# Kernel tuning notes

Hardware: AMD Instinct MI355X
Metric: run time of the kernel (lower is better)

Reference implementation:

```python
import jax, jax.numpy as jnp
import numpy as np
import math

# Config (matches init_kwargs)
H, SQK, PQK, SV, PV = 12, 16, 4, 16, 8
C1, C2 = 384, 128
NR, NA = 512, 256
N = NR + NA
WC = math.sqrt(2.0 / (9.0 * PQK))
WL = math.sqrt(1.0 / 3.0)


def quat_to_rot(q):
    # q: [..., 4] (w, x, y, z); normalize then build rotation matrix [..., 3, 3]
    q = q / jnp.linalg.norm(q, axis=-1, keepdims=True)
    w, x, y, z = q[..., 0], q[..., 1], q[..., 2], q[..., 3]
    return jnp.stack([
        jnp.stack([1 - 2 * (y * y + z * z), 2 * (x * y - w * z), 2 * (x * z + w * y)], -1),
        jnp.stack([2 * (x * y + w * z), 1 - 2 * (x * x + z * z), 2 * (y * z - w * x)], -1),
        jnp.stack([2 * (x * z - w * y), 2 * (y * z + w * x), 1 - 2 * (x * x + y * y)], -1),
    ], -2)


def setup_inputs() -> dict:
    key = jax.random.key(0)
    ks = jax.random.split(key, 16)
    s = 0.02
    return {
        'rec_1d': jax.random.normal(ks[0], (1, NR, C1), jnp.float32),
        'lig_1d': jax.random.normal(ks[1], (1, NA, C1), jnp.float32),
        'rep_2d': jax.random.normal(ks[2], (1, N, N, C2), jnp.float32),
        'rec_T': jax.random.normal(ks[3], (1, NR, 7), jnp.float32),
        'lig_T': jax.random.normal(ks[4], (1, NA, 7), jnp.float32),
        'rec_w1d': jax.random.normal(ks[5], (C1, (2 * SQK + SV) * H), jnp.float32) * s,
        'rec_wpt': jax.random.normal(ks[6], (C1, (2 * PQK + PV) * H * 3), jnp.float32) * s,
        'lig_w1d': jax.random.normal(ks[7], (C1, (2 * SQK + SV) * H), jnp.float32) * s,
        'lig_wpt': jax.random.normal(ks[8], (C1, (2 * PQK + PV) * H * 3), jnp.float32) * s,
        'rr_w': jax.random.normal(ks[9], (C2, H), jnp.float32) * s,
        'll_w': jax.random.normal(ks[10], (C2, H), jnp.float32) * s,
        'rl_w': jax.random.normal(ks[11], (C2, H), jnp.float32) * s,
        'lr_w': jax.random.normal(ks[12], (C2, H), jnp.float32) * s,
        'final_w': jax.random.normal(ks[13], (H * (C2 + SV + 4 * PV), C1), jnp.float32) * s,
        'final_b': jnp.zeros((C1,), jnp.float32),
    }


def reference(rec_1d, lig_1d, rep_2d, rec_T, lig_T, rec_w1d, rec_wpt, lig_w1d, lig_wpt,
              rr_w, ll_w, rl_w, lr_w, final_w, final_b):
    B = rec_1d.shape[0]

    def scalar_kqv(x, w, n):
        kqv = (x @ w).reshape(B, n, H, 2 * SQK + SV)
        return kqv[..., :SQK], kqv[..., SQK:2 * SQK], kqv[..., 2 * SQK:]

    rec_k1, rec_q1, rec_v1 = scalar_kqv(rec_1d, rec_w1d, NR)
    lig_k1, lig_q1, lig_v1 = scalar_kqv(lig_1d, lig_w1d, NA)

    # 2d pair biases per block: [B, i, j, H]
    rr = rep_2d[:, :NR, :NR] @ rr_w
    ll = rep_2d[:, NR:, NR:] @ ll_w
    rl = rep_2d[:, :NR, NR:] @ rl_w
    lr = rep_2d[:, NR:, :NR] @ lr_w

    def point_kqv(x, w, T, n):
        R = quat_to_rot(T[..., :4])          # [B, n, 3, 3]
        t = T[..., 4:]                        # [B, n, 3]
        local = (x @ w).reshape(B, n, 3, H * (2 * PQK + PV))
        glob = jnp.einsum('bnij,bnjd->bnid', R, local) + t[..., None]
        glob = glob.reshape(B, n, 3, H, 2 * PQK + PV)
        return glob[..., :PQK], glob[..., PQK:2 * PQK], glob[..., 2 * PQK:], R, t

    rec_kp, rec_qp, rec_vp, rec_R, rec_t = point_kqv(rec_1d, rec_wpt, rec_T, NR)
    lig_kp, lig_qp, lig_vp, lig_R, lig_t = point_kqv(lig_1d, lig_wpt, lig_T, NA)

    q_point = jnp.concatenate([rec_qp, lig_qp], axis=1)  # [B, N, 3, H, PQK]
    k_point = jnp.concatenate([rec_kp, lig_kp], axis=1)

    # squared distances summed over xyz and points -> [B, N, N, H]
    diff = q_point[:, :, None] - k_point[:, None, :]     # [B, N, N, 3, H, PQK]
    d2 = jnp.sum(jnp.square(diff), axis=3).sum(axis=-1)
    aff = -WC * d2

    bias = jnp.concatenate([
        jnp.concatenate([rr, rl], axis=2),
        jnp.concatenate([lr, ll], axis=2),
    ], axis=1)
    aff = aff + bias

    q1 = jnp.concatenate([rec_q1, lig_q1], axis=1)
    k1 = jnp.concatenate([rec_k1, lig_k1], axis=1)
    aff = aff + (WL / math.sqrt(SQK)) * jnp.einsum('bihc,bjhc->bijh', q1, k1)

    weights = jax.nn.softmax(aff, axis=2)  # [B, N, N, H]

    # 2d aggregation: [B, N, H, C2]
    o_2d = jnp.einsum('bijh,bijc->bihc', weights, rep_2d).reshape(B, N, H * C2)

    # scalar-v term: faithful to source (v_1d.unsqueeze(2) broadcasts over j,
    # so it reduces to v_1d * sum_j weights)
    v_1d = jnp.concatenate([rec_v1, lig_v1], axis=1)     # [B, N, H, SV]
    o_1d = (v_1d * jnp.sum(weights, axis=2)[..., None]).reshape(B, N, H * SV)

    # point-v aggregation in global frame: [B, N, 3, PV, H]
    v_point = jnp.concatenate([rec_vp, lig_vp], axis=1)  # [B, N, 3, H, PV]
    out_global = jnp.einsum('bijh,bjdhp->bidph', weights, v_point)

    def invert(glob, R, t):
        return jnp.einsum('bnji,bnjph->bniph', R, glob - t[..., None, None])

    out_local = jnp.concatenate([
        invert(out_global[:, :NR], rec_R, rec_t),
        invert(out_global[:, NR:], lig_R, lig_t),
    ], axis=1)                                           # [B, N, 3, PV, H]
    out_local = jnp.transpose(out_local, (0, 1, 3, 4, 2))  # [B, N, PV, H, 3]
    o_pt = out_local.reshape(B, N, PV * H * 3)
    o_norm = jnp.sqrt(jnp.sum(jnp.square(out_local), axis=-1)).reshape(B, N, PV * H)

    feat = jnp.concatenate([o_2d, o_1d, o_pt, o_norm], axis=-1)
    return feat @ final_w + final_b
```

## Files before the change

### kernel.cpp

```cpp
#include <hip/hip_runtime.h>
#include <math.h>

#define H_   12
#define NRR  512
#define N_   768
#define C1_  384
#define C2_  128
static __device__ __constant__ float WC_  = 0.2357022603955158f;
static __device__ __constant__ float SC1_ = 0.14433756729740646f;

#define OFF_Q1   0
#define OFF_QP   147456
#define OFF_V1   258048
#define OFF_VP   405504
#define OFF_R    626688
#define OFF_T    633600
#define OFF_KHAT 635904
#define OFF_W    930816
#define OFF_FEAT 8008704
#define OFF_PART 9630720

__global__ __launch_bounds__(192) void proj_kernel(
    const float* __restrict__ rec_1d, const float* __restrict__ lig_1d,
    const float* __restrict__ rec_T,  const float* __restrict__ lig_T,
    const float* __restrict__ rec_w1d, const float* __restrict__ rec_wpt,
    const float* __restrict__ lig_w1d, const float* __restrict__ lig_wpt,
    float* __restrict__ ws) {
  const int tok0 = blockIdx.x * 4;
  const int tid  = threadIdx.x;
  __shared__ float xs[4][384];
  __shared__ float loc[4][576];
  __shared__ float Rs[4][9];
  __shared__ float tts[4][3];

  for (int r = 0; r < 4; ++r) {
    int n = tok0 + r;
    const float* x = (n < NRR) ? rec_1d + n * C1_ : lig_1d + (n - NRR) * C1_;
    for (int k = tid; k < C1_; k += 192) xs[r][k] = x[k];
  }
  if (tid < 4) {
    int n = tok0 + tid;
    const float* T = (n < NRR) ? rec_T + n * 7 : lig_T + (n - NRR) * 7;
    float qw = T[0], qx = T[1], qy = T[2], qz = T[3];
    float inv = 1.0f / sqrtf(qw*qw + qx*qx + qy*qy + qz*qz);
    qw *= inv; qx *= inv; qy *= inv; qz *= inv;
    Rs[tid][0] = 1.f - 2.f*(qy*qy + qz*qz);
    Rs[tid][1] = 2.f*(qx*qy - qw*qz);
    Rs[tid][2] = 2.f*(qx*qz + qw*qy);
    Rs[tid][3] = 2.f*(qx*qy + qw*qz);
    Rs[tid][4] = 1.f - 2.f*(qx*qx + qz*qz);
    Rs[tid][5] = 2.f*(qy*qz - qw*qx);
    Rs[tid][6] = 2.f*(qx*qz - qw*qy);
    Rs[tid][7] = 2.f*(qy*qz + qw*qx);
    Rs[tid][8] = 1.f - 2.f*(qx*qx + qy*qy);
    tts[tid][0] = T[4]; tts[tid][1] = T[5]; tts[tid][2] = T[6];
    float* Rg = ws + OFF_R + n * 9;
    #pragma unroll
    for (int k = 0; k < 9; ++k) Rg[k] = Rs[tid][k];
    float* tg = ws + OFF_T + n * 3;
    tg[0] = T[4]; tg[1] = T[5]; tg[2] = T[6];
  }
  __syncthreads();

  const float* w1 = (tok0 < NRR) ? rec_w1d : lig_w1d;
  const float* w2 = (tok0 < NRR) ? rec_wpt : lig_wpt;
  for (int cc = 0; cc < 3; ++cc) {
    int c = tid + cc * 192;
    float a0=0,a1=0,a2=0,a3=0,b0=0,b1=0,b2=0,b3=0;
    for (int k = 0; k < C1_; ++k) {
      float wv = w1[k * 576 + c];
      float wp = w2[k * 576 + c];
      float x0 = xs[0][k], x1 = xs[1][k], x2 = xs[2][k], x3 = xs[3][k];
      a0 += x0*wv; a1 += x1*wv; a2 += x2*wv; a3 += x3*wv;
      b0 += x0*wp; b1 += x1*wp; b2 += x2*wp; b3 += x3*wp;
    }
    loc[0][c]=b0; loc[1][c]=b1; loc[2][c]=b2; loc[3][c]=b3;
    int h = c / 48, e = c % 48;
    float av[4] = {a0,a1,a2,a3};
    for (int r = 0; r < 4; ++r) {
      int n = tok0 + r;
      if (e < 16)      ws[OFF_KHAT + ((size_t)h*N_ + n)*32 + e] = av[r];
      else if (e < 32) ws[OFF_Q1 + n*192 + h*16 + (e-16)]       = av[r];
      else             ws[OFF_V1 + n*192 + h*16 + (e-32)]       = av[r];
    }
  }
  __syncthreads();

  {
    int cp = tid;
    int h = cp >> 4, e = cp & 15;
    for (int r = 0; r < 4; ++r) {
      int n = tok0 + r;
      float g[3];
      #pragma unroll
      for (int d = 0; d < 3; ++d)
        g[d] = Rs[r][d*3+0]*loc[r][cp] + Rs[r][d*3+1]*loc[r][192+cp]
             + Rs[r][d*3+2]*loc[r][384+cp] + tts[r][d];
      if (e < 4) {
        #pragma unroll
        for (int d = 0; d < 3; ++d)
          ws[OFF_KHAT + ((size_t)h*N_ + n)*32 + 16 + e*3 + d] = g[d];
      } else if (e < 8) {
        #pragma unroll
        for (int d = 0; d < 3; ++d) ws[OFF_QP + n*144 + h*12 + (e-4)*3 + d] = g[d];
      } else {
        #pragma unroll
        for (int d = 0; d < 3; ++d) ws[OFF_VP + n*288 + d*96 + h*8 + (e-8)] = g[d];
      }
    }
  }
}

__global__ __launch_bounds__(256) void bias_kernel(
    const float* __restrict__ rep, const float* __restrict__ rr_w,
    const float* __restrict__ ll_w, const float* __restrict__ rl_w,
    const float* __restrict__ lr_w, float* __restrict__ wsW) {
  const int bx = blockIdx.x;
  const int i = bx / 12, jc = bx % 12;
  const int j0 = jc * 64;
  const int t = threadIdx.x;
  __shared__ float lds[64*128];
  __shared__ float wlw[12*128];
  const float* Wq = (i < NRR) ? ((j0 < NRR) ? rr_w : rl_w)
                              : ((j0 < NRR) ? lr_w : ll_w);
  for (int idx = t; idx < 1536; idx += 256) {
    int h = idx >> 7, c = idx & 127;
    wlw[idx] = Wq[c*12 + h];
  }
  const float* src = rep + ((size_t)i*N_ + j0) * C2_;
  for (int idx = t; idx < 2048; idx += 256) {
    int j = idx >> 5, c4 = idx & 31;
    float4 v = *(const float4*)(src + j*128 + c4*4);
    *(float4*)&lds[j*128 + ((c4 ^ j) & 31) * 4] = v;
  }
  __syncthreads();
  const int j = t & 63, hg = t >> 6;
  const int jx = j & 31;
  float a0 = 0.f, a1 = 0.f, a2 = 0.f;
  const float* w0p = wlw + hg*128;
  const float* w1p = wlw + (hg+4)*128;
  const float* w2p = wlw + (hg+8)*128;
  #pragma unroll 8
  for (int c4 = 0; c4 < 32; ++c4) {
    float4 d  = *(const float4*)&lds[j*128 + ((c4 ^ jx) << 2)];
    float4 w0 = *(const float4*)&w0p[c4*4];
    float4 w1 = *(const float4*)&w1p[c4*4];
    float4 w2 = *(const float4*)&w2p[c4*4];
    a0 += d.x*w0.x + d.y*w0.y + d.z*w0.z + d.w*w0.w;
    a1 += d.x*w1.x + d.y*w1.y + d.z*w1.z + d.w*w1.w;
    a2 += d.x*w2.x + d.y*w2.y + d.z*w2.z + d.w*w2.w;
  }
  wsW[((size_t)i*12 + hg    )*N_ + j0 + j] = a0;
  wsW[((size_t)i*12 + hg + 4)*N_ + j0 + j] = a1;
  wsW[((size_t)i*12 + hg + 8)*N_ + j0 + j] = a2;
}

__global__ __launch_bounds__(256) void attn_kernel(float* ws) {
  const int i = blockIdx.x / H_;
  const int h = blockIdx.x % H_;
  const int tid = threadIdx.x;
  float q1v[16], qpv[12];
  #pragma unroll
  for (int c = 0; c < 16; c += 4)
    *(float4*)&q1v[c] = *(const float4*)(ws + OFF_Q1 + i*192 + h*16 + c);
  #pragma unroll
  for (int c = 0; c < 12; c += 4)
    *(float4*)&qpv[c] = *(const float4*)(ws + OFF_QP + i*144 + h*12 + c);

  float* wrow = ws + OFF_W + ((size_t)i*H_ + h) * N_;
  float aff[3];
  #pragma unroll
  for (int r = 0; r < 3; ++r) {
    int j = tid + r*256;
    const float* khf = ws + OFF_KHAT + ((size_t)h*N_ + j)*32;
    float kv[28];
    #pragma unroll
    for (int c = 0; c < 28; c += 4) *(float4*)&kv[c] = *(const float4*)(khf + c);
    float s = 0.f;
    #pragma unroll
    for (int c = 0; c < 16; ++c) s += q1v[c] * kv[c];
    float d2 = 0.f;
    #pragma unroll
    for (int c = 0; c < 12; ++c) { float df = qpv[c] - kv[16+c]; d2 += df*df; }
    aff[r] = wrow[j] + SC1_*s - WC_*d2;
  }
  float m = fmaxf(fmaxf(aff[0], aff[1]), aff[2]);
  #pragma unroll
  for (int off = 32; off; off >>= 1) m = fmaxf(m, __shfl_xor(m, off));
  __shared__ float redm[4], reds[4];
  int wid = tid >> 6, lane = tid & 63;
  if (lane == 0) redm[wid] = m;
  __syncthreads();
  m = fmaxf(fmaxf(redm[0], redm[1]), fmaxf(redm[2], redm[3]));
  float e0 = __expf(aff[0]-m), e1 = __expf(aff[1]-m), e2 = __expf(aff[2]-m);
  float ssum = e0 + e1 + e2;
  #pragma unroll
  for (int off = 32; off; off >>= 1) ssum += __shfl_xor(ssum, off);
  if (lane == 0) reds[wid] = ssum;
  __syncthreads();
  float invs = 1.0f / (reds[0] + reds[1] + reds[2] + reds[3]);
  wrow[tid      ] = e0 * invs;
  wrow[tid + 256] = e1 * invs;
  wrow[tid + 512] = e2 * invs;
}

__global__ __launch_bounds__(256) void o2d_kernel(
    const float* __restrict__ rep, const float* __restrict__ w,
    float* __restrict__ feat) {
  const int i = blockIdx.x;
  const int t = threadIdx.x;
  __shared__ float wl[N_ * H_];
  for (int idx = t; idx < 2304; idx += 256) {
    float4 g = *(const float4*)(w + (size_t)i*9216 + idx*4);
    int h = idx / 192, j4 = idx % 192;
    wl[(j4*4+0)*12 + h] = g.x;
    wl[(j4*4+1)*12 + h] = g.y;
    wl[(j4*4+2)*12 + h] = g.z;
    wl[(j4*4+3)*12 + h] = g.w;
  }
  __syncthreads();
  const int c4 = t & 31, jg = t >> 5;
  float acc[48];
  #pragma unroll
  for (int k = 0; k < 48; ++k) acc[k] = 0.f;
  const float* rrow = rep + (size_t)i * N_ * C2_;
  #pragma unroll 4
  for (int j = jg; j < N_; j += 8) {
    float4 v = *(const float4*)(rrow + j*128 + c4*4);
    float4 wa = *(const float4*)&wl[j*12];
    float4 wb = *(const float4*)&wl[j*12 + 4];
    float4 wc = *(const float4*)&wl[j*12 + 8];
    float wv[12] = {wa.x,wa.y,wa.z,wa.w, wb.x,wb.y,wb.z,wb.w, wc.x,wc.y,wc.z,wc.w};
    #pragma unroll
    for (int hh = 0; hh < 12; ++hh) {
      acc[hh*4+0] += v.x*wv[hh];
      acc[hh*4+1] += v.y*wv[hh];
      acc[hh*4+2] += v.z*wv[hh];
      acc[hh*4+3] += v.w*wv[hh];
    }
  }
  #pragma unroll
  for (int k = 0; k < 48; ++k) acc[k] += __shfl_xor(acc[k], 32);
  const int wave = t >> 6, lane = t & 63;
  __syncthreads();
  if (wave >= 2 && lane < 32) {
    float* dst = wl + (wave-2)*1536 + lane*48;
    #pragma unroll
    for (int k = 0; k < 48; ++k) dst[k] = acc[k];
  }
  __syncthreads();
  if (wave < 2 && lane < 32) {
    const float* s2 = wl + wave*1536 + lane*48;
    #pragma unroll
    for (int k = 0; k < 48; ++k) acc[k] += s2[k];
  }
  __syncthreads();
  if (wave == 1 && lane < 32) {
    float* dst = wl + lane*48;
    #pragma unroll
    for (int k = 0; k < 48; ++k) dst[k] = acc[k];
  }
  __syncthreads();
  if (wave == 0 && lane < 32) {
    const float* s2 = wl + lane*48;
    #pragma unroll
    for (int k = 0; k < 48; ++k) acc[k] += s2[k];
    #pragma unroll
    for (int hh = 0; hh < 12; ++hh) {
      float4 r;
      r.x = acc[hh*4+0]; r.y = acc[hh*4+1]; r.z = acc[hh*4+2]; r.w = acc[hh*4+3];
      *(float4*)&feat[(size_t)i*2112 + hh*128 + lane*4] = r;
    }
  }
}

__global__ __launch_bounds__(320) void opoint_kernel(
    const float* __restrict__ w, const float* __restrict__ vp,
    const float* __restrict__ R, const float* __restrict__ tvec,
    const float* __restrict__ v1, float* __restrict__ feat) {
  const int i = blockIdx.x;
  const int tid = threadIdx.x;
  __shared__ float wl[H_ * N_];
  __shared__ float og[288];
  __shared__ float ol[288];
  for (int k = tid; k < H_*N_; k += 320) wl[k] = w[(size_t)i*H_*N_ + k];
  __syncthreads();
  if (tid < 288) {
    int d = tid / 96, hh = (tid % 96) / 8;
    float acc = 0.f;
    for (int j = 0; j < N_; ++j) acc += wl[hh*N_ + j] * vp[(size_t)j*288 + tid];
    og[tid] = acc - tvec[i*3 + d];
  }
  if (tid < 192) feat[(size_t)i*2112 + 1536 + tid] = v1[(size_t)i*192 + tid];
  __syncthreads();
  if (tid < 288) {
    int i3 = tid / 96, rem = tid % 96, hh = rem / 8, p = rem % 8;
    float o = R[i*9 + 0*3 + i3] * og[0*96 + rem]
            + R[i*9 + 1*3 + i3] * og[1*96 + rem]
            + R[i*9 + 2*3 + i3] * og[2*96 + rem];
    ol[tid] = o;
    feat[(size_t)i*2112 + 1728 + p*36 + hh*3 + i3] = o;
  }
  __syncthreads();
  if (tid < 96) {
    int hh = tid / 8, p = tid % 8;
    float a = ol[0*96 + tid], b = ol[1*96 + tid], c = ol[2*96 + tid];
    feat[(size_t)i*2112 + 2016 + p*12 + hh] = sqrtf(a*a + b*b + c*c);
  }
}

__global__ __launch_bounds__(384) void final1_kernel(
    const float* __restrict__ ws, const float* __restrict__ fw,
    float* __restrict__ part) {
  const int i0 = blockIdx.x * 4;
  const int ks = blockIdx.y;
  const int o  = threadIdx.x;
  const int k0 = ks * 1056;
  __shared__ float fl[4 * 1056];
  const float* feat = ws + OFF_FEAT;
  for (int idx = o; idx < 1056; idx += 384) {
    int r = idx / 264, f4 = idx % 264;
    *(float4*)&fl[r*1056 + f4*4] =
        *(const float4*)(feat + (size_t)(i0+r)*2112 + k0 + f4*4);
  }
  __syncthreads();
  float a0=0,a1=0,a2=0,a3=0;
  for (int f4 = 0; f4 < 264; ++f4) {
    int f = k0 + f4*4;
    float w0 = fw[(size_t)(f+0)*384 + o];
    float w1 = fw[(size_t)(f+1)*384 + o];
    float w2 = fw[(size_t)(f+2)*384 + o];
    float w3 = fw[(size_t)(f+3)*384 + o];
    float4 f0 = *(const float4*)&fl[0*1056 + f4*4];
    float4 f1 = *(const float4*)&fl[1*1056 + f4*4];
    float4 f2 = *(const float4*)&fl[2*1056 + f4*4];
    float4 f3 = *(const float4*)&fl[3*1056 + f4*4];
    a0 += f0.x*w0 + f0.y*w1 + f0.z*w2 + f0.w*w3;
    a1 += f1.x*w0 + f1.y*w1 + f1.z*w2 + f1.w*w3;
    a2 += f2.x*w0 + f2.y*w1 + f2.z*w2 + f2.w*w3;
    a3 += f3.x*w0 + f3.y*w1 + f3.z*w2 + f3.w*w3;
  }
  part[((size_t)ks*N_ + i0+0)*384 + o] = a0;
  part[((size_t)ks*N_ + i0+1)*384 + o] = a1;
  part[((size_t)ks*N_ + i0+2)*384 + o] = a2;
  part[((size_t)ks*N_ + i0+3)*384 + o] = a3;
}

__global__ __launch_bounds__(256) void final2_kernel(
    const float* __restrict__ part, const float* __restrict__ fb,
    float* __restrict__ out) {
  int idx = blockIdx.x * 256 + threadIdx.x;
  int col = idx % 384;
  out[idx] = part[idx] + part[294912 + idx] + fb[col];
}

extern "C" void kernel_launch(void* const* d_in, const int* in_sizes, int n_in,
                              void* d_out, int out_size, void* d_ws, size_t ws_size,
                              hipStream_t stream) {
  const float* rec_1d  = (const float*)d_in[0];
  const float* lig_1d  = (const float*)d_in[1];
  const float* rep_2d  = (const float*)d_in[2];
  const float* rec_T   = (const float*)d_in[3];
  const float* lig_T   = (const float*)d_in[4];
  const float* rec_w1d = (const float*)d_in[5];
  const float* rec_wpt = (const float*)d_in[6];
  const float* lig_w1d = (const float*)d_in[7];
  const float* lig_wpt = (const float*)d_in[8];
  const float* rr_w    = (const float*)d_in[9];
  const float* ll_w    = (const float*)d_in[10];
  const float* rl_w    = (const float*)d_in[11];
  const float* lr_w    = (const float*)d_in[12];
  const float* final_w = (const float*)d_in[13];
  const float* final_b = (const float*)d_in[14];
  float* ws  = (float*)d_ws;
  float* out = (float*)d_out;

  proj_kernel<<<192, 192, 0, stream>>>(rec_1d, lig_1d, rec_T, lig_T,
                                       rec_w1d, rec_wpt, lig_w1d, lig_wpt, ws);
  bias_kernel<<<N_*12, 256, 0, stream>>>(rep_2d, rr_w, ll_w, rl_w, lr_w,
                                         ws + OFF_W);
  attn_kernel<<<N_*H_, 256, 0, stream>>>(ws);
  o2d_kernel<<<N_, 256, 0, stream>>>(rep_2d, ws + OFF_W, ws + OFF_FEAT);
  opoint_kernel<<<N_, 320, 0, stream>>>(ws + OFF_W, ws + OFF_VP, ws + OFF_R,
                                        ws + OFF_T, ws + OFF_V1, ws + OFF_FEAT);
  final1_kernel<<<dim3(N_/4, 2), 384, 0, stream>>>(ws, final_w, ws + OFF_PART);
  final2_kernel<<<1152, 256, 0, stream>>>(ws + OFF_PART, final_b, out);
}
```

Baseline: 863.9 us.

## Fuse bias, softmax and o2d into a single-pass flash-style kernel with bf16 MFMA

New measurement: 986.6 us. 14.2% more time.

```diff
diff --git a/kernel.cpp b/kernel.cpp
--- a/kernel.cpp
+++ b/kernel.cpp
@@ -9,16 +9,32 @@
 static __device__ __constant__ float WC_  = 0.2357022603955158f;
 static __device__ __constant__ float SC1_ = 0.14433756729740646f;
 
-#define OFF_Q1   0
-#define OFF_QP   147456
-#define OFF_V1   258048
-#define OFF_VP   405504
-#define OFF_R    626688
-#define OFF_T    633600
-#define OFF_KHAT 635904
-#define OFF_W    930816
-#define OFF_FEAT 8008704
-#define OFF_PART 9630720
+#define OFF_Q1     0
+#define OFF_QP     147456
+#define OFF_V1     258048
+#define OFF_VP     405504
+#define OFF_R      626688
+#define OFF_T      633600
+#define OFF_KHAT   635904
+#define OFF_WFRAG  930816
+#define OFF_QKF    934912
+#define OFF_MUSED  10372096
+#define OFF_MSFIN  10519552
+#define OFF_W      10544128
+#define OFF_FEAT   17622016
+#define OFF_PART   19244032
+
+typedef __attribute__((ext_vector_type(8))) short short8_m;
+typedef __attribute__((ext_vector_type(4))) float f32x4_m;
+
+__device__ __forceinline__ ushort f2bf(float f) {
+  uint u = __float_as_uint(f);
+  uint r = (u + 0x7fffu + ((u >> 16) & 1u)) >> 16;
+  return (ushort)r;
+}
+__device__ __forceinline__ float bf2f(ushort v) {
+  return __uint_as_float(((uint)v) << 16);
+}
 
 __global__ __launch_bounds__(192) void proj_kernel(
     const float* __restrict__ rec_1d, const float* __restrict__ lig_1d,
@@ -111,179 +127,254 @@
   }
 }
 
-__global__ __launch_bounds__(256) void bias_kernel(
-    const float* __restrict__ rep, const float* __restrict__ rr_w,
-    const float* __restrict__ ll_w, const float* __restrict__ rl_w,
-    const float* __restrict__ lr_w, float* __restrict__ wsW) {
-  const int bx = blockIdx.x;
-  const int i = bx / 12, jc = bx % 12;
-  const int j0 = jc * 64;
+__global__ __launch_bounds__(256) void wfrag_kernel(
+    const float* __restrict__ rr_w, const float* __restrict__ rl_w,
+    const float* __restrict__ lr_w, const float* __restrict__ ll_w,
+    float* __restrict__ ws) {
+  ushort* wf = (ushort*)(ws + OFF_WFRAG);
+  const float* mats[4] = { rr_w, rl_w, lr_w, ll_w };
+  for (int idx = threadIdx.x; idx < 8192; idx += 256) {
+    int mat = idx >> 11;
+    int r   = idx & 2047;
+    int ks  = r >> 9;
+    int r2  = r & 511;
+    int l   = r2 >> 3;
+    int e   = r2 & 7;
+    int n   = l & 15;
+    int k   = ks*32 + (l>>4)*8 + e;
+    float v = (n < 12) ? mats[mat][k*12 + n] : 0.f;
+    wf[idx] = f2bf(v);
+  }
+}
+
+__global__ __launch_bounds__(256) void qk_kernel(float* __restrict__ ws) {
+  const int b = blockIdx.x;
+  const int i = b / 12, tile = b % 12;
   const int t = threadIdx.x;
-  __shared__ float lds[64*128];
-  __shared__ float wlw[12*128];
-  const float* Wq = (i < NRR) ? ((j0 < NRR) ? rr_w : rl_w)
-                              : ((j0 < NRR) ? lr_w : ll_w);
-  for (int idx = t; idx < 1536; idx += 256) {
-    int h = idx >> 7, c = idx & 127;
-    wlw[idx] = Wq[c*12 + h];
-  }
-  const float* src = rep + ((size_t)i*N_ + j0) * C2_;
-  for (int idx = t; idx < 2048; idx += 256) {
-    int j = idx >> 5, c4 = idx & 31;
-    float4 v = *(const float4*)(src + j*128 + c4*4);
-    *(float4*)&lds[j*128 + ((c4 ^ j) & 31) * 4] = v;
-  }
-  __syncthreads();
-  const int j = t & 63, hg = t >> 6;
-  const int jx = j & 31;
-  float a0 = 0.f, a1 = 0.f, a2 = 0.f;
-  const float* w0p = wlw + hg*128;
-  const float* w1p = wlw + (hg+4)*128;
-  const float* w2p = wlw + (hg+8)*128;
-  #pragma unroll 8
-  for (int c4 = 0; c4 < 32; ++c4) {
-    float4 d  = *(const float4*)&lds[j*128 + ((c4 ^ jx) << 2)];
-    float4 w0 = *(const float4*)&w0p[c4*4];
-    float4 w1 = *(const float4*)&w1p[c4*4];
-    float4 w2 = *(const float4*)&w2p[c4*4];
-    a0 += d.x*w0.x + d.y*w0.y + d.z*w0.z + d.w*w0.w;
-    a1 += d.x*w1.x + d.y*w1.y + d.z*w1.z + d.w*w1.w;
-    a2 += d.x*w2.x + d.y*w2.y + d.z*w2.z + d.w*w2.w;
-  }
-  wsW[((size_t)i*12 + hg    )*N_ + j0 + j] = a0;
-  wsW[((size_t)i*12 + hg + 4)*N_ + j0 + j] = a1;
-  wsW[((size_t)i*12 + hg + 8)*N_ + j0 + j] = a2;
-}
-
-__global__ __launch_bounds__(256) void attn_kernel(float* ws) {
-  const int i = blockIdx.x / H_;
-  const int h = blockIdx.x % H_;
-  const int tid = threadIdx.x;
-  float q1v[16], qpv[12];
-  #pragma unroll
-  for (int c = 0; c < 16; c += 4)
-    *(float4*)&q1v[c] = *(const float4*)(ws + OFF_Q1 + i*192 + h*16 + c);
-  #pragma unroll
-  for (int c = 0; c < 12; c += 4)
-    *(float4*)&qpv[c] = *(const float4*)(ws + OFF_QP + i*144 + h*12 + c);
-
-  float* wrow = ws + OFF_W + ((size_t)i*H_ + h) * N_;
-  float aff[3];
-  #pragma unroll
-  for (int r = 0; r < 3; ++r) {
-    int j = tid + r*256;
-    const float* khf = ws + OFF_KHAT + ((size_t)h*N_ + j)*32;
-    float kv[28];
-    #pragma unroll
-    for (int c = 0; c < 28; c += 4) *(float4*)&kv[c] = *(const float4*)(khf + c);
-    float s = 0.f;
-    #pragma unroll
-    for (int c = 0; c < 16; ++c) s += q1v[c] * kv[c];
-    float d2 = 0.f;
-    #pragma unroll
-    for (int c = 0; c < 12; ++c) { float df = qpv[c] - kv[16+c]; d2 += df*df; }
-    aff[r] = wrow[j] + SC1_*s - WC_*d2;
-  }
-  float m = fmaxf(fmaxf(aff[0], aff[1]), aff[2]);
-  #pragma unroll
-  for (int off = 32; off; off >>= 1) m = fmaxf(m, __shfl_xor(m, off));
-  __shared__ float redm[4], reds[4];
-  int wid = tid >> 6, lane = tid & 63;
-  if (lane == 0) redm[wid] = m;
-  __syncthreads();
-  m = fmaxf(fmaxf(redm[0], redm[1]), fmaxf(redm[2], redm[3]));
-  float e0 = __expf(aff[0]-m), e1 = __expf(aff[1]-m), e2 = __expf(aff[2]-m);
-  float ssum = e0 + e1 + e2;
-  #pragma unroll
-  for (int off = 32; off; off >>= 1) ssum += __shfl_xor(ssum, off);
-  if (lane == 0) reds[wid] = ssum;
-  __syncthreads();
-  float invs = 1.0f / (reds[0] + reds[1] + reds[2] + reds[3]);
-  wrow[tid      ] = e0 * invs;
-  wrow[tid + 256] = e1 * invs;
-  wrow[tid + 512] = e2 * invs;
-}
-
-__global__ __launch_bounds__(256) void o2d_kernel(
-    const float* __restrict__ rep, const float* __restrict__ w,
-    float* __restrict__ feat) {
+  const int l = t & 63, w = t >> 6;
+  __shared__ float q1s[12][16];
+  __shared__ float qps[12][12];
+  if (t < 192) q1s[t >> 4][t & 15] = ws[OFF_Q1 + i*192 + t];
+  if (t < 144) qps[t / 12][t % 12] = ws[OFF_QP + i*144 + t];
+  __syncthreads();
+  const int h = l & 15, jq = l >> 4;
+  float val[4] = {0.f, 0.f, 0.f, 0.f};
+  if (h < 12) {
+    #pragma unroll
+    for (int rr = 0; rr < 4; ++rr) {
+      int j = tile*64 + w*16 + jq*4 + rr;
+      const float* kf = ws + OFF_KHAT + ((size_t)h*N_ + j)*32;
+      float kv[28];
+      #pragma unroll
+      for (int c = 0; c < 28; c += 4) *(float4*)&kv[c] = *(const float4*)(kf + c);
+      float s = 0.f;
+      #pragma unroll
+      for (int c = 0; c < 16; ++c) s += q1s[h][c] * kv[c];
+      float d2 = 0.f;
+      #pragma unroll
+      for (int d = 0; d < 12; ++d) { float df = qps[h][d] - kv[16+d]; d2 += df*df; }
+      val[rr] = SC1_*s - WC_*d2;
+    }
+  }
+  float4 o; o.x = val[0]; o.y = val[1]; o.z = val[2]; o.w = val[3];
+  *(float4*)(ws + OFF_QKF + ((size_t)b*4 + w)*256 + l*4) = o;
+}
+
+__global__ __launch_bounds__(256) void flash_kernel(
+    const float* __restrict__ rep, float* __restrict__ ws) {
   const int i = blockIdx.x;
   const int t = threadIdx.x;
-  __shared__ float wl[N_ * H_];
-  for (int idx = t; idx < 2304; idx += 256) {
-    float4 g = *(const float4*)(w + (size_t)i*9216 + idx*4);
-    int h = idx / 192, j4 = idx % 192;
-    wl[(j4*4+0)*12 + h] = g.x;
-    wl[(j4*4+1)*12 + h] = g.y;
-    wl[(j4*4+2)*12 + h] = g.z;
-    wl[(j4*4+3)*12 + h] = g.w;
-  }
-  __syncthreads();
-  const int c4 = t & 31, jg = t >> 5;
+  const int lane = t & 63, wv = t >> 6;
+  __shared__ ushort A[64 * 128];
+  __shared__ ushort e_l[64 * 16];
+  __shared__ float mt[64], est[64], fact[16], mrun[16], srun[16];
+
+  const short8_m* wf = (const short8_m*)(ws + OFF_WFRAG);
+  const int m0 = (i < NRR) ? 0 : 2, m1 = (i < NRR) ? 1 : 3;
+  short8_m bf0[4], bf1[4];
+  #pragma unroll
+  for (int ks = 0; ks < 4; ++ks) {
+    bf0[ks] = wf[(m0*4 + ks)*64 + lane];
+    bf1[ks] = wf[(m1*4 + ks)*64 + lane];
+  }
+  if (t < 16) { mrun[t] = -1e30f; srun[t] = 0.f; }
   float acc[48];
   #pragma unroll
   for (int k = 0; k < 48; ++k) acc[k] = 0.f;
-  const float* rrow = rep + (size_t)i * N_ * C2_;
-  #pragma unroll 4
-  for (int j = jg; j < N_; j += 8) {
-    float4 v = *(const float4*)(rrow + j*128 + c4*4);
-    float4 wa = *(const float4*)&wl[j*12];
-    float4 wb = *(const float4*)&wl[j*12 + 4];
-    float4 wc = *(const float4*)&wl[j*12 + 8];
-    float wv[12] = {wa.x,wa.y,wa.z,wa.w, wb.x,wb.y,wb.z,wb.w, wc.x,wc.y,wc.z,wc.w};
-    #pragma unroll
-    for (int hh = 0; hh < 12; ++hh) {
-      acc[hh*4+0] += v.x*wv[hh];
-      acc[hh*4+1] += v.y*wv[hh];
-      acc[hh*4+2] += v.z*wv[hh];
-      acc[hh*4+3] += v.w*wv[hh];
-    }
+
+  const int cq = t & 31, jgr = t >> 5;
+  const int hh = lane & 15, jq = lane >> 4;
+  const int rowA = wv*16 + hh;
+  __syncthreads();
+
+  for (int tile = 0; tile < 12; ++tile) {
+    const float* src = rep + ((size_t)i*N_ + tile*64) * C2_;
+    #pragma unroll
+    for (int k = 0; k < 8; ++k) {
+      int j = jgr + k*8;
+      float4 v = *(const float4*)(src + j*C2_ + cq*4);
+      uint2 p;
+      p.x = (uint)f2bf(v.x) | ((uint)f2bf(v.y) << 16);
+      p.y = (uint)f2bf(v.z) | ((uint)f2bf(v.w) << 16);
+      int slot = (cq >> 1) ^ (j & 7);
+      *(uint2*)((char*)A + j*256 + slot*16 + (cq & 1)*8) = p;
+    }
+    __syncthreads();
+
+    f32x4_m c4 = {0.f, 0.f, 0.f, 0.f};
+    #pragma unroll
+    for (int ks = 0; ks < 4; ++ks) {
+      int slot = (ks*4 + jq) ^ (rowA & 7);
+      short8_m a = *(const short8_m*)((const char*)A + rowA*256 + slot*16);
+      c4 = __builtin_amdgcn_mfma_f32_16x16x32_bf16(
+          a, (tile < 8) ? bf0[ks] : bf1[ks], c4, 0, 0, 0);
+    }
+    float4 qk4 = *(const float4*)(ws + OFF_QKF +
+        (((size_t)i*12 + tile)*4 + wv)*256 + lane*4);
+    float aff0 = c4[0] + qk4.x, aff1 = c4[1] + qk4.y;
+    float aff2 = c4[2] + qk4.z, aff3 = c4[3] + qk4.w;
+
+    float ml = fmaxf(fmaxf(aff0, aff1), fmaxf(aff2, aff3));
+    ml = fmaxf(ml, __shfl_xor(ml, 16));
+    ml = fmaxf(ml, __shfl_xor(ml, 32));
+    if (jq == 0) mt[wv*16 + hh] = ml;
+    __syncthreads();
+    if (t < 12) {
+      float m4 = fmaxf(fmaxf(mt[t], mt[16+t]), fmaxf(mt[32+t], mt[48+t]));
+      float mn = fmaxf(mrun[t], m4);
+      fact[t]  = __expf(mrun[t] - mn);
+      mrun[t]  = mn;
+      ws[OFF_MUSED + (size_t)i*192 + tile*16 + t] = mn;
+    }
+    __syncthreads();
+
+    const bool valid = (hh < 12);
+    float mh = valid ? mrun[hh] : 0.f;
+    float e0 = valid ? __expf(aff0 - mh) : 0.f;
+    float e1 = valid ? __expf(aff1 - mh) : 0.f;
+    float e2 = valid ? __expf(aff2 - mh) : 0.f;
+    float e3 = valid ? __expf(aff3 - mh) : 0.f;
+    if (valid) {
+      int jb = wv*16 + jq*4;
+      e_l[(jb+0)*16 + hh] = f2bf(e0);
+      e_l[(jb+1)*16 + hh] = f2bf(e1);
+      e_l[(jb+2)*16 + hh] = f2bf(e2);
+      e_l[(jb+3)*16 + hh] = f2bf(e3);
+    }
+    float es = e0 + e1 + e2 + e3;
+    es += __shfl_xor(es, 16);
+    es += __shfl_xor(es, 32);
+    if (jq == 0) est[wv*16 + hh] = es;
+    __syncthreads();
+    if (t < 12)
+      srun[t] = srun[t]*fact[t] + (est[t] + est[16+t] + est[32+t] + est[48+t]);
+
+    float fc[12];
+    #pragma unroll
+    for (int h = 0; h < 12; ++h) fc[h] = fact[h];
+    #pragma unroll
+    for (int h = 0; h < 12; ++h) {
+      acc[h*4+0] *= fc[h]; acc[h*4+1] *= fc[h];
+      acc[h*4+2] *= fc[h]; acc[h*4+3] *= fc[h];
+    }
+    #pragma unroll
+    for (int k = 0; k < 8; ++k) {
+      int j = jgr + k*8;
+      const char* ep = (const char*)e_l + j*32;
+      uint4 u4 = *(const uint4*)ep;
+      uint2 u2 = *(const uint2*)(ep + 16);
+      float ef[12];
+      ef[0] = __uint_as_float(u4.x << 16); ef[1] = __uint_as_float(u4.x & 0xffff0000u);
+      ef[2] = __uint_as_float(u4.y << 16); ef[3] = __uint_as_float(u4.y & 0xffff0000u);
+      ef[4] = __uint_as_float(u4.z << 16); ef[5] = __uint_as_float(u4.z & 0xffff0000u);
+      ef[6] = __uint_as_float(u4.w << 16); ef[7] = __uint_as_float(u4.w & 0xffff0000u);
+      ef[8] = __uint_as_float(u2.x << 16); ef[9] = __uint_as_float(u2.x & 0xffff0000u);
+      ef[10] = __uint_as_float(u2.y << 16); ef[11] = __uint_as_float(u2.y & 0xffff0000u);
+      int slot = (cq >> 1) ^ (j & 7);
+      uint2 av = *(const uint2*)((const char*)A + j*256 + slot*16 + (cq & 1)*8);
+      float af[4];
+      af[0] = __uint_as_float(av.x << 16); af[1] = __uint_as_float(av.x & 0xffff0000u);
+      af[2] = __uint_as_float(av.y << 16); af[3] = __uint_as_float(av.y & 0xffff0000u);
+      #pragma unroll
+      for (int h = 0; h < 12; ++h) {
+        acc[h*4+0] += ef[h]*af[0];
+        acc[h*4+1] += ef[h]*af[1];
+        acc[h*4+2] += ef[h]*af[2];
+        acc[h*4+3] += ef[h]*af[3];
+      }
+    }
+    #pragma unroll
+    for (int k = 0; k < 3; ++k) {
+      int h = wv + k*4;
+      ws[OFF_W + (size_t)i*9216 + h*768 + tile*64 + lane] =
+          bf2f(e_l[lane*16 + h]);
+    }
+    __syncthreads();
+  }
+
+  if (t < 12) {
+    ws[OFF_MSFIN + i*32 + t]      = mrun[t];
+    ws[OFF_MSFIN + i*32 + 16 + t] = srun[t];
   }
   #pragma unroll
   for (int k = 0; k < 48; ++k) acc[k] += __shfl_xor(acc[k], 32);
-  const int wave = t >> 6, lane = t & 63;
-  __syncthreads();
-  if (wave >= 2 && lane < 32) {
-    float* dst = wl + (wave-2)*1536 + lane*48;
+  float* scr = (float*)A;
+  __syncthreads();
+  if (wv >= 2 && lane < 32) {
+    float* dst = scr + (wv-2)*1536 + lane*48;
     #pragma unroll
     for (int k = 0; k < 48; ++k) dst[k] = acc[k];
   }
   __syncthreads();
-  if (wave < 2 && lane < 32) {
-    const float* s2 = wl + wave*1536 + lane*48;
+  if (wv < 2 && lane < 32) {
+    const float* s2 = scr + wv*1536 + lane*48;
     #pragma unroll
     for (int k = 0; k < 48; ++k) acc[k] += s2[k];
   }
   __syncthreads();
-  if (wave == 1 && lane < 32) {
-    float* dst = wl + lane*48;
+  if (wv == 1 && lane < 32) {
+    float* dst = scr + lane*48;
     #pragma unroll
     for (int k = 0; k < 48; ++k) dst[k] = acc[k];
   }
   __syncthreads();
-  if (wave == 0 && lane < 32) {
-    const float* s2 = wl + lane*48;
+  if (wv == 0 && lane < 32) {
+    const float* s2 = scr + lane*48;
     #pragma unroll
     for (int k = 0; k < 48; ++k) acc[k] += s2[k];
-    #pragma unroll
-    for (int hh = 0; hh < 12; ++hh) {
+    float* feat = ws + OFF_FEAT + (size_t)i*2112;
+    #pragma unroll
+    for (int h = 0; h < 12; ++h) {
+      float inv = 1.0f / srun[h];
       float4 r;
-      r.x = acc[hh*4+0]; r.y = acc[hh*4+1]; r.z = acc[hh*4+2]; r.w = acc[hh*4+3];
-      *(float4*)&feat[(size_t)i*2112 + hh*128 + lane*4] = r;
+      r.x = acc[h*4+0]*inv; r.y = acc[h*4+1]*inv;
+      r.z = acc[h*4+2]*inv; r.w = acc[h*4+3]*inv;
+      *(float4*)&feat[h*128 + lane*4] = r;
     }
   }
 }
 
 __global__ __launch_bounds__(320) void opoint_kernel(
-    const float* __restrict__ w, const float* __restrict__ vp,
+    const float* __restrict__ ws_w, const float* __restrict__ vp,
     const float* __restrict__ R, const float* __restrict__ tvec,
-    const float* __restrict__ v1, float* __restrict__ feat) {
+    const float* __restrict__ v1, const float* __restrict__ mused,
+    const float* __restrict__ msfin, float* __restrict__ feat) {
   const int i = blockIdx.x;
   const int tid = threadIdx.x;
   __shared__ float wl[H_ * N_];
+  __shared__ float cf[144];
   __shared__ float og[288];
   __shared__ float ol[288];
-  for (int k = tid; k < H_*N_; k += 320) wl[k] = w[(size_t)i*H_*N_ + k];
+  if (tid < 144) {
+    int h = tid / 12, tl = tid % 12;
+    float sfin = msfin[i*32 + 16 + h];
+    cf[tid] = __expf(mused[(size_t)i*192 + tl*16 + h] - msfin[i*32 + h]) / sfin;
+  }
+  __syncthreads();
+  for (int k = tid; k < H_*N_; k += 320) {
+    int h = k / 768, j = k - h*768;
+    wl[k] = ws_w[(size_t)i*9216 + k] * cf[h*12 + (j >> 6)];
+  }
   __syncthreads();
   if (tid < 288) {
     int d = tid / 96, hh = (tid % 96) / 8;
@@ -377,12 +468,12 @@
 
   proj_kernel<<<192, 192, 0, stream>>>(rec_1d, lig_1d, rec_T, lig_T,
                                        rec_w1d, rec_wpt, lig_w1d, lig_wpt, ws);
-  bias_kernel<<<N_*12, 256, 0, stream>>>(rep_2d, rr_w, ll_w, rl_w, lr_w,
-                                         ws + OFF_W);
-  attn_kernel<<<N_*H_, 256, 0, stream>>>(ws);
-  o2d_kernel<<<N_, 256, 0, stream>>>(rep_2d, ws + OFF_W, ws + OFF_FEAT);
+  wfrag_kernel<<<1, 256, 0, stream>>>(rr_w, rl_w, lr_w, ll_w, ws);
+  qk_kernel<<<N_*12, 256, 0, stream>>>(ws);
+  flash_kernel<<<N_, 256, 0, stream>>>(rep_2d, ws);
   opoint_kernel<<<N_, 320, 0, stream>>>(ws + OFF_W, ws + OFF_VP, ws + OFF_R,
-                                        ws + OFF_T, ws + OFF_V1, ws + OFF_FEAT);
+                                        ws + OFF_T, ws + OFF_V1, ws + OFF_MUSED,
+                                        ws + OFF_MSFIN, ws + OFF_FEAT);
   final1_kernel<<<dim3(N_/4, 2), 384, 0, stream>>>(ws, final_w, ws + OFF_PART);
   final2_kernel<<<1152, 256, 0, stream>>>(ws + OFF_PART, final_b, out);
 }
```
